# Performance work log

Hardware: AMD Instinct MI355X
Metric: run time of the kernel (lower is better)

Reference implementation:

```python
import math
import jax, jax.numpy as jnp
import numpy as np
from jax import lax

B, L, C_IN = 8, 1024, 64
D_MODEL, N_HEADS, D_FF, E_LAYERS, FACTOR = 512, 8, 2048, 3, 5


def conv1d_circ(x, w):
    # x [B,L,Cin], w [Cout,Cin,K]; torch Conv1d with padding_mode='circular'
    pad = (w.shape[-1] - 1) // 2
    xp = jnp.pad(x, ((0, 0), (pad, pad), (0, 0)), mode='wrap')
    return lax.conv_general_dilated(xp, jnp.transpose(w, (2, 1, 0)), (1,), 'VALID',
                                    dimension_numbers=('NWC', 'WIO', 'NWC'))


def pos_emb(Lq, d):
    pos = jnp.arange(Lq, dtype=jnp.float32)[:, None]
    div = jnp.exp(jnp.arange(0, d, 2, dtype=jnp.float32) * (-math.log(10000.0) / d))
    pe = jnp.zeros((Lq, d), dtype=jnp.float32)
    pe = pe.at[:, 0::2].set(jnp.sin(pos * div)).at[:, 1::2].set(jnp.cos(pos * div))
    return pe


def layer_norm(x, g, b, eps=1e-5):
    m = x.mean(-1, keepdims=True)
    v = ((x - m) ** 2).mean(-1, keepdims=True)
    return (x - m) / jnp.sqrt(v + eps) * g + b


def prob_attention(Q, K, V, rkey):
    # ProbSparse self-attention (mask_flag=False). Q,K,V: [B,H,L,D]
    Bq, H, Lq, D = Q.shape
    U = min(FACTOR * int(math.ceil(math.log(Lq))), Lq)  # sample_k == n_top since L_Q == L_K
    idx = jax.random.randint(rkey, (Lq, U), 0, Lq)       # per-query sampled key indices
    Ks = jnp.take(K, idx, axis=2)                        # [B,H,L,U,D]
    QKs = jnp.einsum('bhld,bhlud->bhlu', Q, Ks)          # sampled scores
    M = QKs.max(-1) - QKs.sum(-1) / Lq                   # sparsity measure (sum / L_K)
    _, top = lax.top_k(M, U)                             # [B,H,U] top-u query indices
    Qr = jnp.take_along_axis(Q, top[..., None], axis=2)  # [B,H,U,D]
    scores = jnp.einsum('bhud,bhld->bhul', Qr, K) * (1.0 / math.sqrt(D))
    attn = jax.nn.softmax(scores, axis=-1)
    upd = jnp.einsum('bhul,bhld->bhud', attn, V)
    # initial context = mean of V broadcast over queries; scatter updates at top-u
    ctx = jnp.broadcast_to(V.mean(axis=2, keepdims=True), (Bq, H, Lq, D))
    bi = jnp.arange(Bq)[:, None, None]
    hi = jnp.arange(H)[None, :, None]
    ctx = ctx.at[bi, hi, top].set(upd)
    return ctx


def attn_block(x, Wq, bq, Wk, bk, Wv, bv, Wo, bo, rkey):
    Bq, Lq, Dm = x.shape
    Dh = Dm // N_HEADS
    q = (x @ Wq.T + bq).reshape(Bq, Lq, N_HEADS, Dh).transpose(0, 2, 1, 3)
    k = (x @ Wk.T + bk).reshape(Bq, Lq, N_HEADS, Dh).transpose(0, 2, 1, 3)
    v = (x @ Wv.T + bv).reshape(Bq, Lq, N_HEADS, Dh).transpose(0, 2, 1, 3)
    ctx = prob_attention(q, k, v, rkey)
    out = ctx.transpose(0, 2, 1, 3).reshape(Bq, Lq, Dm)
    return out @ Wo.T + bo


def distil_conv(x, w, b, g, be):
    # Conv1d(k=3, circular) -> BatchNorm1d (batch stats) -> ELU -> MaxPool1d(3,2,1)
    y = conv1d_circ(x, w) + b
    mu = y.mean((0, 1))
    var = ((y - mu) ** 2).mean((0, 1))
    y = (y - mu) / jnp.sqrt(var + 1e-5) * g + be
    y = jax.nn.elu(y)
    y = lax.reduce_window(y, -jnp.inf, lax.max, (1, 3, 1), (1, 2, 1),
                          ((0, 0), (1, 1), (0, 0)))
    return y


def forward(x_enc, tok_w, Wq, bq, Wk, bk, Wv, bv, Wo, bo, c1w, c1b, c2w, c2b,
            n1g, n1b, n2g, n2b, dcw, dcb, bng, bnb, fng, fnb):
    x = x_enc + 1e-10
    x = conv1d_circ(x, tok_w) + pos_emb(x.shape[1], D_MODEL)  # embedding (dropout=0)
    for l in range(E_LAYERS):
        rkey = jax.random.fold_in(jax.random.key(42), l)
        x = x + attn_block(x, Wq[l], bq[l], Wk[l], bk[l], Wv[l], bv[l], Wo[l], bo[l], rkey)
        y = x = layer_norm(x, n1g[l], n1b[l])
        y = jax.nn.relu(y @ c1w[l].T + c1b[l])   # Conv1d k=1 == linear
        y = y @ c2w[l].T + c2b[l]
        x = layer_norm(x + y, n2g[l], n2b[l])
        if l < E_LAYERS - 1:
            x = distil_conv(x, dcw[l], dcb[l], bng[l], bnb[l])
    x = layer_norm(x, fng, fnb)
    return x.mean(axis=1)  # [B, D_MODEL]


def setup_inputs() -> dict:
    key = jax.random.key(0)
    ks = jax.random.split(key, 12)
    s = 0.02
    E = E_LAYERS
    return {
        'x_enc': jax.random.normal(ks[0], (B, L, C_IN), jnp.float32),
        'tok_w': jax.random.normal(ks[1], (D_MODEL, C_IN, 3), jnp.float32) * s,
        'Wq': jax.random.normal(ks[2], (E, D_MODEL, D_MODEL), jnp.float32) * s,
        'bq': jnp.zeros((E, D_MODEL), jnp.float32),
        'Wk': jax.random.normal(ks[3], (E, D_MODEL, D_MODEL), jnp.float32) * s,
        'bk': jnp.zeros((E, D_MODEL), jnp.float32),
        'Wv': jax.random.normal(ks[4], (E, D_MODEL, D_MODEL), jnp.float32) * s,
        'bv': jnp.zeros((E, D_MODEL), jnp.float32),
        'Wo': jax.random.normal(ks[5], (E, D_MODEL, D_MODEL), jnp.float32) * s,
        'bo': jnp.zeros((E, D_MODEL), jnp.float32),
        'c1w': jax.random.normal(ks[6], (E, D_FF, D_MODEL), jnp.float32) * s,
        'c1b': jnp.zeros((E, D_FF), jnp.float32),
        'c2w': jax.random.normal(ks[7], (E, D_MODEL, D_FF), jnp.float32) * s,
        'c2b': jnp.zeros((E, D_MODEL), jnp.float32),
        'n1g': jnp.ones((E, D_MODEL), jnp.float32),
        'n1b': jnp.zeros((E, D_MODEL), jnp.float32),
        'n2g': jnp.ones((E, D_MODEL), jnp.float32),
        'n2b': jnp.zeros((E, D_MODEL), jnp.float32),
        'dcw': jax.random.normal(ks[8], (E - 1, D_MODEL, D_MODEL, 3), jnp.float32) * s,
        'dcb': jnp.zeros((E - 1, D_MODEL), jnp.float32),
        'bng': jnp.ones((E - 1, D_MODEL), jnp.float32),
        'bnb': jnp.zeros((E - 1, D_MODEL), jnp.float32),
        'fng': jnp.ones((D_MODEL,), jnp.float32),
        'fnb': jnp.zeros((D_MODEL,), jnp.float32),
    }


def reference(x_enc, tok_w, Wq, bq, Wk, bk, Wv, bv, Wo, bo, c1w, c1b, c2w, c2b,
              n1g, n1b, n2g, n2b, dcw, dcb, bng, bnb, fng, fnb):
    return forward(x_enc, tok_w, Wq, bq, Wk, bk, Wv, bv, Wo, bo, c1w, c1b, c2w, c2b,
                   n1g, n1b, n2g, n2b, dcw, dcb, bng, bnb, fng, fnb)
```

## Files before the change

kernel.cpp:

```cpp
#include <hip/hip_runtime.h>
#include <hip/hip_bf16.h>
#include <math.h>

typedef __hip_bfloat16 bf16;
typedef short bf16x8 __attribute__((ext_vector_type(8)));
typedef float f32x4 __attribute__((ext_vector_type(4)));

__device__ inline short f2bs(float x) {
  bf16 h = __float2bfloat16(x);
  return *reinterpret_cast<short*>(&h);
}

__device__ inline void gload16(const bf16* g, bf16* l) {
  __builtin_amdgcn_global_load_lds(
      (const __attribute__((address_space(1))) unsigned int*)g,
      (__attribute__((address_space(3))) unsigned int*)l, 16, 0, 0);
}

__device__ inline void threefry2x32(unsigned k0, unsigned k1,
                                    unsigned x0, unsigned x1,
                                    unsigned& o0, unsigned& o1) {
  unsigned ks[3] = {k0, k1, k0 ^ k1 ^ 0x1BD11BDAu};
  const int rot[2][4] = {{13, 15, 26, 6}, {17, 29, 16, 24}};
  x0 += ks[0];
  x1 += ks[1];
  #pragma unroll
  for (int i = 0; i < 5; i++) {
    const int* r = rot[i & 1];
    #pragma unroll
    for (int j = 0; j < 4; j++) {
      x0 += x1;
      x1 = (x1 << r[j]) | (x1 >> (32 - r[j]));
      x1 ^= x0;
    }
    x0 += ks[(i + 1) % 3];
    x1 += ks[(i + 2) % 3] + (unsigned)(i + 1);
  }
  o0 = x0;
  o1 = x1;
}

__global__ void idx_kernel(int* __restrict__ idx, int L, int U, int layer) {
  int total = L * U, half = total / 2;
  int i = blockIdx.x * blockDim.x + threadIdx.x;
  if (i >= half) return;
  unsigned k0, k1;
  threefry2x32(0u, 42u, 0u, (unsigned)layer, k0, k1);
  unsigned o0, o1;
  threefry2x32(k0, k1, (unsigned)i, (unsigned)(half + i), o0, o1);
  idx[i] = (int)(o0 & (unsigned)(L - 1));
  idx[half + i] = (int)(o1 & (unsigned)(L - 1));
}

__global__ __launch_bounds__(256) void bgemm_g(
    const bf16* __restrict__ A, const bf16* __restrict__ W,
    const float* __restrict__ bias, const float* __restrict__ R, int rmod,
    float* __restrict__ C, bf16* __restrict__ Cb,
    int M, int N, int K, int relu, int outmode) {
  __shared__ bf16 As[2][64 * 64];
  __shared__ bf16 Ws[2][64 * 64];
  int tid = threadIdx.x;
  int lane = tid & 63, w = tid >> 6;
  size_t row0 = (size_t)blockIdx.x * 64, col0 = (size_t)blockIdx.y * 64;
  int srow = w * 16 + (lane >> 3);
  int scol = (((lane & 7) ^ (lane >> 3)) << 4) >> 1;
  const bf16* agA0 = A + (row0 + srow) * K + scol;
  const bf16* agA1 = A + (row0 + srow + 8) * K + scol;
  const bf16* agW0 = W + (col0 + srow) * K + scol;
  const bf16* agW1 = W + (col0 + srow + 8) * K + scol;
  int db0 = (w * 16) * 64;
  int db1 = (w * 16 + 8) * 64;
  int wr = (w >> 1) << 5, wc = (w & 1) << 5;
  int fr = lane & 15;
  int fkb = ((lane >> 4) << 3) << 1;
  f32x4 acc[2][2] = {};
  int nt = K >> 6;
  gload16(agA0, As[0] + db0); gload16(agA1, As[0] + db1);
  gload16(agW0, Ws[0] + db0); gload16(agW1, Ws[0] + db1);
  int cur = 0;
  for (int t = 0; t < nt; t++) {
    __syncthreads();
    if (t + 1 < nt) {
      int ko = (t + 1) << 6;
      gload16(agA0 + ko, As[cur ^ 1] + db0); gload16(agA1 + ko, As[cur ^ 1] + db1);
      gload16(agW0 + ko, Ws[cur ^ 1] + db0); gload16(agW1 + ko, Ws[cur ^ 1] + db1);
    }
    const char* ab = (const char*)As[cur];
    const char* wb = (const char*)Ws[cur];
    bf16x8 af[2][2], bfv[2][2];
    #pragma unroll
    for (int m = 0; m < 2; m++) {
      int row = wr + m * 16 + fr;
      int xr = (row & 7) << 4;
      #pragma unroll
      for (int kk = 0; kk < 2; kk++)
        af[m][kk] = *(const bf16x8*)(ab + row * 128 + ((fkb + kk * 64) ^ xr));
    }
    #pragma unroll
    for (int n = 0; n < 2; n++) {
      int row = wc + n * 16 + fr;
      int xr = (row & 7) << 4;
      #pragma unroll
      for (int kk = 0; kk < 2; kk++)
        bfv[n][kk] = *(const bf16x8*)(wb + row * 128 + ((fkb + kk * 64) ^ xr));
    }
    #pragma unroll
    for (int m = 0; m < 2; m++)
      #pragma unroll
      for (int n = 0; n < 2; n++) {
        acc[m][n] = __builtin_amdgcn_mfma_f32_16x16x32_bf16(af[m][0], bfv[n][0], acc[m][n], 0, 0, 0);
        acc[m][n] = __builtin_amdgcn_mfma_f32_16x16x32_bf16(af[m][1], bfv[n][1], acc[m][n], 0, 0, 0);
      }
    cur ^= 1;
  }
  int cr = (lane >> 4) << 2;
  int cc0 = lane & 15;
  #pragma unroll
  for (int m = 0; m < 2; m++) {
    #pragma unroll
    for (int n = 0; n < 2; n++) {
      #pragma unroll
      for (int r = 0; r < 4; r++) {
        size_t rr = row0 + wr + m * 16 + cr + r;
        size_t cc = col0 + wc + n * 16 + cc0;
        float v = acc[m][n][r];
        if (bias) v += bias[cc];
        if (R) v += rmod ? R[(rr % rmod) * N + cc] : R[rr * N + cc];
        if (relu) v = fmaxf(v, 0.f);
        if (outmode != 2) C[rr * N + cc] = v;
        if (outmode) Cb[rr * N + cc] = __float2bfloat16(v);
      }
    }
  }
}

__global__ void castw_kernel(const float* __restrict__ wq, const float* __restrict__ wk,
                             const float* __restrict__ wv, const float* __restrict__ wo,
                             const float* __restrict__ c1, const float* __restrict__ c2,
                             bf16* __restrict__ wqkv, bf16* __restrict__ wob,
                             bf16* __restrict__ c1b, bf16* __restrict__ c2b) {
  int i = blockIdx.x * 256 + threadIdx.x;
  if (i >= 786432) return;
  const float* s;
  bf16* d;
  int j;
  if (i < 196608) {
    s = (i < 65536) ? wq : (i < 131072) ? wk : wv;
    float4 v = ((const float4*)s)[i & 65535];
    d = wqkv + (size_t)i * 4;
    d[0] = __float2bfloat16(v.x); d[1] = __float2bfloat16(v.y);
    d[2] = __float2bfloat16(v.z); d[3] = __float2bfloat16(v.w);
    return;
  }
  if (i < 262144) { s = wo; j = i - 196608; d = wob + (size_t)j * 4; }
  else if (i < 524288) { s = c1; j = i - 262144; d = c1b + (size_t)j * 4; }
  else { s = c2; j = i - 524288; d = c2b + (size_t)j * 4; }
  float4 v = ((const float4*)s)[j];
  d[0] = __float2bfloat16(v.x); d[1] = __float2bfloat16(v.y);
  d[2] = __float2bfloat16(v.z); d[3] = __float2bfloat16(v.w);
}

__global__ void catb3_kernel(const float* __restrict__ a, const float* __restrict__ b,
                             const float* __restrict__ c, float* __restrict__ d) {
  int i = blockIdx.x * 256 + threadIdx.x;
  if (i >= 1536) return;
  d[i] = (i < 512) ? a[i] : (i < 1024) ? b[i - 512] : c[i - 1024];
}

__global__ void wperm_kernel(const float* __restrict__ w, bf16* __restrict__ wcol) {
  int i = blockIdx.x * 256 + threadIdx.x;
  if (i >= 512 * 1536) return;
  int o = i / 1536, r = i % 1536, k = r / 512, c = r % 512;
  wcol[i] = __float2bfloat16(w[o * 1536 + c * 3 + k]);
}

__global__ void tokperm_kernel(const float* __restrict__ w, bf16* __restrict__ d) {
  int i = blockIdx.x * 256 + threadIdx.x;
  if (i >= 512 * 192) return;
  int o = i / 192, r = i % 192, k = r / 64, c = r % 64;
  d[i] = __float2bfloat16(w[o * 192 + c * 3 + k]);
}

__global__ void pe_kernel(float* __restrict__ PE) {
  int t = blockIdx.x, o = threadIdx.x;
  int i2 = o >> 1;
  float div = expf((float)(2 * i2) * (-9.210340371976184f / 512.f));
  float ang = (float)t * div;
  PE[t * 512 + o] = (o & 1) ? cosf(ang) : sinf(ang);
}

__global__ void im2col_e_kernel(const float* __restrict__ x, bf16* __restrict__ d,
                                int B, int L) {
  size_t i = (size_t)blockIdx.x * 256 + threadIdx.x;
  if (i >= (size_t)B * L * 192) return;
  int j = (int)(i % 192);
  size_t row = i / 192;
  int k = j >> 6, c = j & 63;
  int t = (int)(row % L), b = (int)(row / L);
  int ts = (t - 1 + k) & (L - 1);
  d[i] = __float2bfloat16(x[((size_t)(b * L + ts)) * 64 + c] + 1e-10f);
}

__global__ __launch_bounds__(256) void sparsity_kernel(
    const float* __restrict__ QKV, const int* __restrict__ idx,
    float* __restrict__ M, int B, int H, int L, int U) {
  int tpb = L >> 2;
  int xcd = blockIdx.x & 7, slot = blockIdx.x >> 3;
  int bh = xcd + ((slot / tpb) << 3);
  int tb = slot % tpb;
  int wave = threadIdx.x >> 6;
  int t = tb * 4 + wave;
  int lane = threadIdx.x & 63;
  int h = bh & 7, b = bh >> 3;
  int ul = lane >> 3;
  int j = lane & 7;
  const float* qrow = QKV + ((size_t)(b * L + t)) * 1536 + h * 64 + j * 8;
  float4 qa = *(const float4*)qrow;
  float4 qb = *(const float4*)(qrow + 4);
  const float* kbase = QKV + (size_t)b * L * 1536 + 512 + h * 64 + j * 8;
  const int* irow = idx + t * U;
  float mx = -INFINITY, sm = 0.f;
  int iters = (U + 7) >> 3;
  for (int i = 0; i < iters; i++) {
    int u = i * 8 + ul;
    bool valid = (u < U);
    int kt = valid ? irow[u] : 0;
    const float* kr = kbase + (size_t)kt * 1536;
    float4 ka = *(const float4*)kr;
    float4 kb = *(const float4*)(kr + 4);
    float part = qa.x * ka.x + qa.y * ka.y + qa.z * ka.z + qa.w * ka.w +
                 qb.x * kb.x + qb.y * kb.y + qb.z * kb.z + qb.w * kb.w;
    #pragma unroll
    for (int off = 1; off < 8; off <<= 1) part += __shfl_xor(part, off);
    if (valid) { mx = fmaxf(mx, part); sm += part; }
  }
  #pragma unroll
  for (int off = 8; off < 64; off <<= 1) {
    mx = fmaxf(mx, __shfl_xor(mx, off));
    sm += __shfl_xor(sm, off);
  }
  if (lane == 0) M[(size_t)bh * L + t] = mx - sm / (float)L;
}

__global__ __launch_bounds__(1024) void topk_kernel(
    const float* __restrict__ M, int* __restrict__ top, int L, int U) {
  __shared__ float wv[16];
  __shared__ int wi[16];
  __shared__ int best_s;
  int bh = blockIdx.x, tid = threadIdx.x;
  int lane = tid & 63, w = tid >> 6;
  float v = (tid < L) ? M[(size_t)bh * L + tid] : -INFINITY;
  int myt = tid;
  for (int it = 0; it < U; it++) {
    float bv = v;
    int bi = myt;
    #pragma unroll
    for (int off = 32; off; off >>= 1) {
      float ov = __shfl_xor(bv, off);
      int oi = __shfl_xor(bi, off);
      if (ov > bv || (ov == bv && oi < bi)) { bv = ov; bi = oi; }
    }
    if (lane == 0) { wv[w] = bv; wi[w] = bi; }
    __syncthreads();
    if (w == 0) {
      float v2 = (lane < 16) ? wv[lane] : -INFINITY;
      int i2 = (lane < 16) ? wi[lane] : 0x7fffffff;
      #pragma unroll
      for (int off = 8; off; off >>= 1) {
        float ov = __shfl_xor(v2, off);
        int oi = __shfl_xor(i2, off);
        if (ov > v2 || (ov == v2 && oi < i2)) { v2 = ov; i2 = oi; }
      }
      if (lane == 0) { best_s = i2; top[bh * U + it] = i2; }
    }
    __syncthreads();
    if (myt == best_s) v = -INFINITY;
  }
}

__global__ __launch_bounds__(512) void vmean_part_kernel(
    const float* __restrict__ QKV, float* __restrict__ VP, int L, int segs) {
  int b = blockIdx.x, s = blockIdx.y, c = threadIdx.x;
  int per = L / segs;
  const float* vb = QKV + ((size_t)(b * L + s * per)) * 1536 + 1024 + c;
  float acc = 0.f;
  for (int t = 0; t < per; t++) acc += vb[(size_t)t * 1536];
  VP[((size_t)(b * segs + s)) * 512 + c] = acc;
}

__global__ void vmean_reduce_kernel(const float* __restrict__ VP, float* __restrict__ Vmean,
                                    int segs, int L) {
  int i = blockIdx.x * 256 + threadIdx.x;
  if (i >= 8 * 512) return;
  int b = i >> 9, c = i & 511;
  float acc = 0.f;
  for (int s = 0; s < segs; s++) acc += VP[((size_t)(b * segs + s)) * 512 + c];
  Vmean[i] = acc / (float)L;
}

__global__ void bcast_ctx_kernel(const float* __restrict__ Vmean, bf16* __restrict__ ATTb,
                                 int B, int L) {
  size_t i = (size_t)blockIdx.x * 256 + threadIdx.x;
  if (i >= (size_t)B * L * 512) return;
  int c = (int)(i % 512);
  int b = (int)(i / ((size_t)512 * L));
  ATTb[i] = __float2bfloat16(Vmean[b * 512 + c]);
}

__global__ __launch_bounds__(256) void attn_mfma_kernel(
    const float* __restrict__ QKV, const int* __restrict__ top,
    bf16* __restrict__ ATTb, int B, int H, int L, int U) {
  __shared__ short q_lds[64 * 72];
  __shared__ short k_lds[64 * 72];
  __shared__ short vt_lds[64 * 72];
  __shared__ short p_lds[4][16 * 72];
  int bh = blockIdx.x;
  int h = bh & 7, b = bh >> 3;
  int tid = threadIdx.x;
  int lane = tid & 63, w = tid >> 6;
  int r = tid >> 2, q4 = tid & 3, c0 = q4 << 4;
  int fr = lane & 15, fk = (lane >> 4) << 3, g = lane >> 4;

  {
    short tmp[16];
    if (r < U) {
      int tq = top[bh * U + r];
      const float* src = QKV + ((size_t)(b * L + tq)) * 1536 + h * 64 + c0;
      #pragma unroll
      for (int i = 0; i < 4; i++) {
        float4 v = ((const float4*)src)[i];
        tmp[i * 4 + 0] = f2bs(v.x); tmp[i * 4 + 1] = f2bs(v.y);
        tmp[i * 4 + 2] = f2bs(v.z); tmp[i * 4 + 3] = f2bs(v.w);
      }
    } else {
      #pragma unroll
      for (int i = 0; i < 16; i++) tmp[i] = 0;
    }
    *(bf16x8*)&q_lds[r * 72 + c0] = *(bf16x8*)&tmp[0];
    *(bf16x8*)&q_lds[r * 72 + c0 + 8] = *(bf16x8*)&tmp[8];
  }
  __syncthreads();
  bf16x8 aq0 = *(const bf16x8*)&q_lds[(w * 16 + fr) * 72 + fk];
  bf16x8 aq1 = *(const bf16x8*)&q_lds[(w * 16 + fr) * 72 + 32 + fk];

  f32x4 ctx[4] = {};
  float m_run[4], l_run[4];
  #pragma unroll
  for (int i = 0; i < 4; i++) { m_run[i] = -INFINITY; l_run[i] = 0.f; }

  for (int t0 = 0; t0 < L; t0 += 64) {
    __syncthreads();
    {
      const float* ks = QKV + ((size_t)(b * L + t0 + r)) * 1536 + 512 + h * 64 + c0;
      const float* vs = ks + 512;
      short kt[16];
      #pragma unroll
      for (int i = 0; i < 4; i++) {
        float4 v = ((const float4*)ks)[i];
        kt[i * 4 + 0] = f2bs(v.x); kt[i * 4 + 1] = f2bs(v.y);
        kt[i * 4 + 2] = f2bs(v.z); kt[i * 4 + 3] = f2bs(v.w);
      }
      *(bf16x8*)&k_lds[r * 72 + c0] = *(bf16x8*)&kt[0];
      *(bf16x8*)&k_lds[r * 72 + c0 + 8] = *(bf16x8*)&kt[8];
      #pragma unroll
      for (int i = 0; i < 4; i++) {
        float4 v = ((const float4*)vs)[i];
        vt_lds[(c0 + i * 4 + 0) * 72 + r] = f2bs(v.x);
        vt_lds[(c0 + i * 4 + 1) * 72 + r] = f2bs(v.y);
        vt_lds[(c0 + i * 4 + 2) * 72 + r] = f2bs(v.z);
        vt_lds[(c0 + i * 4 + 3) * 72 + r] = f2bs(v.w);
      }
    }
    __syncthreads();
    f32x4 s[4];
    #pragma unroll
    for (int n = 0; n < 4; n++) {
      bf16x8 b0 = *(const bf16x8*)&k_lds[(n * 16 + fr) * 72 + fk];
      bf16x8 b1 = *(const bf16x8*)&k_lds[(n * 16 + fr) * 72 + 32 + fk];
      f32x4 z = {};
      z = __builtin_amdgcn_mfma_f32_16x16x32_bf16(aq0, b0, z, 0, 0, 0);
      s[n] = __builtin_amdgcn_mfma_f32_16x16x32_bf16(aq1, b1, z, 0, 0, 0);
    }
    #pragma unroll
    for (int n = 0; n < 4; n++)
      #pragma unroll
      for (int rg = 0; rg < 4; rg++) s[n][rg] *= 0.125f;
    #pragma unroll
    for (int rg = 0; rg < 4; rg++) {
      float tm = fmaxf(fmaxf(s[0][rg], s[1][rg]), fmaxf(s[2][rg], s[3][rg]));
      #pragma unroll
      for (int off = 1; off < 16; off <<= 1) tm = fmaxf(tm, __shfl_xor(tm, off));
      float mnew = fmaxf(m_run[rg], tm);
      float sc_old = expf(m_run[rg] - mnew);
      float rowsum = 0.f;
      #pragma unroll
      for (int n = 0; n < 4; n++) {
        float p = expf(s[n][rg] - mnew);
        s[n][rg] = p;
        rowsum += p;
      }
      #pragma unroll
      for (int off = 1; off < 16; off <<= 1) rowsum += __shfl_xor(rowsum, off);
      l_run[rg] = l_run[rg] * sc_old + rowsum;
      m_run[rg] = mnew;
      #pragma unroll
      for (int nd = 0; nd < 4; nd++) ctx[nd][rg] *= sc_old;
    }
    short* pw = p_lds[w];
    #pragma unroll
    for (int n = 0; n < 4; n++)
      #pragma unroll
      for (int rg = 0; rg < 4; rg++)
        pw[(g * 4 + rg) * 72 + n * 16 + fr] = f2bs(s[n][rg]);
    bf16x8 pa0 = *(const bf16x8*)&pw[fr * 72 + fk];
    bf16x8 pa1 = *(const bf16x8*)&pw[fr * 72 + 32 + fk];
    #pragma unroll
    for (int nd = 0; nd < 4; nd++) {
      bf16x8 v0 = *(const bf16x8*)&vt_lds[(nd * 16 + fr) * 72 + fk];
      bf16x8 v1 = *(const bf16x8*)&vt_lds[(nd * 16 + fr) * 72 + 32 + fk];
      ctx[nd] = __builtin_amdgcn_mfma_f32_16x16x32_bf16(pa0, v0, ctx[nd], 0, 0, 0);
      ctx[nd] = __builtin_amdgcn_mfma_f32_16x16x32_bf16(pa1, v1, ctx[nd], 0, 0, 0);
    }
  }
  #pragma unroll
  for (int rg = 0; rg < 4; rg++) {
    int qq = w * 16 + g * 4 + rg;
    if (qq < U) {
      int tq = top[bh * U + qq];
      float inv = 1.f / l_run[rg];
      #pragma unroll
      for (int nd = 0; nd < 4; nd++) {
        int d = nd * 16 + fr;
        ATTb[((size_t)(b * L + tq)) * 512 + h * 64 + d] =
            __float2bfloat16(ctx[nd][rg] * inv);
      }
    }
  }
}

__global__ __launch_bounds__(256) void ln_kernel(
    const float* __restrict__ Xin, const float* __restrict__ g,
    const float* __restrict__ bta, float* __restrict__ Xout,
    bf16* __restrict__ Xoutb, int rows) {
  __shared__ float part[8];
  int r = blockIdx.x, tid = threadIdx.x;
  int lane = tid & 63, w = tid >> 6;
  const float* xr = Xin + (size_t)r * 512;
  float v0 = xr[tid], v1 = xr[tid + 256];
  float s = v0 + v1;
  #pragma unroll
  for (int off = 1; off < 64; off <<= 1) s += __shfl_xor(s, off);
  if (lane == 0) part[w] = s;
  __syncthreads();
  float mean = (part[0] + part[1] + part[2] + part[3]) * (1.f / 512.f);
  float d0 = v0 - mean, d1 = v1 - mean;
  float q = d0 * d0 + d1 * d1;
  #pragma unroll
  for (int off = 1; off < 64; off <<= 1) q += __shfl_xor(q, off);
  if (lane == 0) part[4 + w] = q;
  __syncthreads();
  float var = (part[4] + part[5] + part[6] + part[7]) * (1.f / 512.f);
  float rs = rsqrtf(var + 1e-5f);
  float o0 = d0 * rs * g[tid] + bta[tid];
  float o1 = d1 * rs * g[tid + 256] + bta[tid + 256];
  float* out = Xout + (size_t)r * 512;
  out[tid] = o0;
  out[tid + 256] = o1;
  if (Xoutb) {
    Xoutb[(size_t)r * 512 + tid] = __float2bfloat16(o0);
    Xoutb[(size_t)r * 512 + tid + 256] = __float2bfloat16(o1);
  }
}

__global__ void im2col_kernel(const float* __restrict__ X, bf16* __restrict__ XCOL,
                              int B, int L) {
  size_t i = (size_t)blockIdx.x * 256 + threadIdx.x;
  size_t total = (size_t)B * L * 1536;
  if (i >= total) return;
  int c = (int)(i % 512);
  int k = (int)((i / 512) % 3);
  size_t row = i / 1536;
  int t = (int)(row % L), b = (int)(row / L);
  int ts = (t - 1 + k + L) % L;
  XCOL[i] = __float2bfloat16(X[((size_t)(b * L + ts)) * 512 + c]);
}

__global__ void zero_kernel(float* p, int n) {
  int i = blockIdx.x * 256 + threadIdx.x;
  if (i < n) p[i] = 0.f;
}

__global__ __launch_bounds__(256) void bnstat_kernel(
    const float* __restrict__ Y, float* __restrict__ acc, int rows) {
  int tid = threadIdx.x;
  int c0 = tid, c1 = tid + 256;
  float s0 = 0, s1 = 0, q0 = 0, q1 = 0;
  for (int r = blockIdx.x; r < rows; r += gridDim.x) {
    float v0 = Y[(size_t)r * 512 + c0];
    float v1 = Y[(size_t)r * 512 + c1];
    s0 += v0; q0 += v0 * v0;
    s1 += v1; q1 += v1 * v1;
  }
  atomicAdd(&acc[c0], s0);
  atomicAdd(&acc[c1], s1);
  atomicAdd(&acc[512 + c0], q0);
  atomicAdd(&acc[512 + c1], q1);
}

__global__ void bnpool_kernel(const float* __restrict__ Y, const float* __restrict__ acc,
                              const float* __restrict__ g, const float* __restrict__ be,
                              float* __restrict__ Xout, bf16* __restrict__ Xoutb,
                              int B, int L, int rows) {
  int Lout = L / 2;
  size_t i = (size_t)blockIdx.x * 256 + threadIdx.x;
  if (i >= (size_t)B * Lout * 512) return;
  int c = (int)(i % 512);
  size_t orow = i / 512;
  int to = (int)(orow % Lout), b = (int)(orow / Lout);
  float mu = acc[c] / (float)rows;
  float var = acc[512 + c] / (float)rows - mu * mu;
  float rs = rsqrtf(var + 1e-5f) * g[c];
  float mx = -INFINITY;
  #pragma unroll
  for (int dj = -1; dj <= 1; dj++) {
    int j = 2 * to + dj;
    if (j < 0 || j >= L) continue;
    float v = (Y[((size_t)(b * L + j)) * 512 + c] - mu) * rs + be[c];
    v = v > 0.f ? v : expm1f(v);
    mx = fmaxf(mx, v);
  }
  Xout[i] = mx;
  Xoutb[i] = __float2bfloat16(mx);
}

__global__ void meanrows_part_kernel(const float* __restrict__ Xin, float* __restrict__ MP,
                                     int L, int segs) {
  int b = blockIdx.x, s = blockIdx.y, d = threadIdx.x;
  int per = L / segs;
  const float* base = Xin + ((size_t)(b * L + s * per)) * 512 + d;
  float acc = 0.f;
  for (int t = 0; t < per; t++) acc += base[(size_t)t * 512];
  MP[((size_t)(b * segs + s)) * 512 + d] = acc;
}

__global__ void meanrows_red_kernel(const float* __restrict__ MP, float* __restrict__ out,
                                    int segs, int L) {
  int i = blockIdx.x * 256 + threadIdx.x;
  if (i >= 8 * 512) return;
  int b = i >> 9, c = i & 511;
  float acc = 0.f;
  for (int s = 0; s < segs; s++) acc += MP[((size_t)(b * segs + s)) * 512 + c];
  out[i] = acc / (float)L;
}

extern "C" void kernel_launch(void* const* d_in, const int* in_sizes, int n_in,
                              void* d_out, int out_size, void* d_ws, size_t ws_size,
                              hipStream_t stream) {
  const float* x_enc = (const float*)d_in[0];
  const float* tok_w = (const float*)d_in[1];
  const float* Wq = (const float*)d_in[2];
  const float* bq = (const float*)d_in[3];
  const float* Wk = (const float*)d_in[4];
  const float* bk = (const float*)d_in[5];
  const float* Wv = (const float*)d_in[6];
  const float* bv = (const float*)d_in[7];
  const float* Wo = (const float*)d_in[8];
  const float* bo = (const float*)d_in[9];
  const float* c1w = (const float*)d_in[10];
  const float* c1b = (const float*)d_in[11];
  const float* c2w = (const float*)d_in[12];
  const float* c2b = (const float*)d_in[13];
  const float* n1g = (const float*)d_in[14];
  const float* n1b = (const float*)d_in[15];
  const float* n2g = (const float*)d_in[16];
  const float* n2b = (const float*)d_in[17];
  const float* dcw = (const float*)d_in[18];
  const float* dcb = (const float*)d_in[19];
  const float* bng = (const float*)d_in[20];
  const float* bnb = (const float*)d_in[21];
  const float* fng = (const float*)d_in[22];
  const float* fnb = (const float*)d_in[23];

  const int B = 8, H = 8;
  const size_t NX = 4194304;

  float* ws = (float*)d_ws;
  float* X    = ws;
  float* XLN  = ws + NX;
  float* QKVf = ws + 2 * NX;
  bf16* H2b   = (bf16*)(ws + 2 * NX);
  float* Yc   = ws + 2 * NX;
  bf16* XCOLb = (bf16*)(ws + 4 * NX);
  bf16* INb   = (bf16*)(ws + 5 * NX);
  bf16* ATTb  = (bf16*)(ws + 5 * NX + NX / 2);
  float* WB   = ws + 6 * NX;
  bf16* WQKVb = (bf16*)(WB);
  bf16* Wob  = (bf16*)(WB + 393216);
  bf16* c1wb = (bf16*)(WB + 524288);
  bf16* c2wb = (bf16*)(WB + 1048576);
  bf16* wcvb = (bf16*)(WB + 1572864);
  bf16* tokwb = (bf16*)(WB + 1966080);
  float* PE   = WB + 2015232;
  float* MBUF = PE + 524288;
  float* VMEAN = MBUF + 65536;
  float* BNACC = VMEAN + 4096;
  int* IDX = (int*)(BNACC + 1024);
  int* TOP = IDX + 35840;
  float* VPART = (float*)(TOP + 2240);
  float* BQKV = VPART + 131072;

  pe_kernel<<<1024, 512, 0, stream>>>(PE);
  tokperm_kernel<<<(512 * 192 + 255) / 256, 256, 0, stream>>>(tok_w, tokwb);
  im2col_e_kernel<<<(int)(((size_t)B * 1024 * 192 + 255) / 256), 256, 0, stream>>>(
      x_enc, INb, B, 1024);
  bgemm_g<<<dim3(128, 8), 256, 0, stream>>>(INb, tokwb, nullptr, PE, 1024,
                                            X, INb, 8192, 512, 192, 0, 1);

  int L = 1024;
  for (int l = 0; l < 3; l++) {
    int U = (L == 256) ? 30 : 35;
    int rows = B * L;
    dim3 g64(rows / 64, 8);

    castw_kernel<<<3072, 256, 0, stream>>>(
        Wq + (size_t)l * 262144, Wk + (size_t)l * 262144, Wv + (size_t)l * 262144,
        Wo + (size_t)l * 262144, c1w + (size_t)l * 1048576, c2w + (size_t)l * 1048576,
        WQKVb, Wob, c1wb, c2wb);
    catb3_kernel<<<6, 256, 0, stream>>>(bq + l * 512, bk + l * 512, bv + l * 512, BQKV);
    if (l < 2)
      wperm_kernel<<<3072, 256, 0, stream>>>(dcw + (size_t)l * 786432, wcvb);

    bgemm_g<<<dim3(rows / 64, 24), 256, 0, stream>>>(
        INb, WQKVb, BQKV, nullptr, 0, QKVf, nullptr, rows, 1536, 512, 0, 0);

    int half = L * U / 2;
    idx_kernel<<<(half + 255) / 256, 256, 0, stream>>>(IDX, L, U, l);
    sparsity_kernel<<<(B * H * L) / 4, 256, 0, stream>>>(QKVf, IDX, MBUF, B, H, L, U);
    topk_kernel<<<B * H, 1024, 0, stream>>>(MBUF, TOP, L, U);
    vmean_part_kernel<<<dim3(B, 32), 512, 0, stream>>>(QKVf, VPART, L, 32);
    vmean_reduce_kernel<<<16, 256, 0, stream>>>(VPART, VMEAN, 32, L);
    bcast_ctx_kernel<<<(rows * 512) / 256, 256, 0, stream>>>(VMEAN, ATTb, B, L);
    attn_mfma_kernel<<<B * H, 256, 0, stream>>>(QKVf, TOP, ATTb, B, H, L, U);

    bgemm_g<<<g64, 256, 0, stream>>>(ATTb, Wob, bo + l * 512, X, 0,
                                     X, nullptr, rows, 512, 512, 0, 0);
    ln_kernel<<<rows, 256, 0, stream>>>(X, n1g + l * 512, n1b + l * 512, XLN, INb, rows);
    bgemm_g<<<dim3(rows / 64, 32), 256, 0, stream>>>(
        INb, c1wb, c1b + l * 2048, nullptr, 0, nullptr, H2b, rows, 2048, 512, 1, 2);
    bgemm_g<<<g64, 256, 0, stream>>>(H2b, c2wb, c2b + l * 512, XLN, 0,
                                     X, nullptr, rows, 512, 2048, 0, 0);
    ln_kernel<<<rows, 256, 0, stream>>>(X, n2g + l * 512, n2b + l * 512, X, nullptr, rows);

    if (l < 2) {
      im2col_kernel<<<(int)(((size_t)rows * 1536) / 256), 256, 0, stream>>>(X, XCOLb, B, L);
      bgemm_g<<<g64, 256, 0, stream>>>(XCOLb, wcvb, dcb + l * 512, nullptr, 0,
                                       Yc, nullptr, rows, 512, 1536, 0, 0);
      zero_kernel<<<4, 256, 0, stream>>>(BNACC, 1024);
      bnstat_kernel<<<128, 256, 0, stream>>>(Yc, BNACC, rows);
      bnpool_kernel<<<(rows / 2 * 512) / 256, 256, 0, stream>>>(
          Yc, BNACC, bng + l * 512, bnb + l * 512, X, INb, B, L, rows);
      L >>= 1;
    }
  }

  int rowsF = B * L;
  ln_kernel<<<rowsF, 256, 0, stream>>>(X, fng, fnb, XLN, nullptr, rowsF);
  meanrows_part_kernel<<<dim3(8, 8), 512, 0, stream>>>(XLN, VPART, L, 8);
  meanrows_red_kernel<<<16, 256, 0, stream>>>(VPART, (float*)d_out, 8, L);
}
```

Baseline: 877.2 us.

## Split ProbSparse attention over key chunks with a separate combine kernel

The attention kernel used to launch only B*H=64 blocks, each sweeping every key, which leaves most CUs idle. It now splits the key range into SPLIT chunks (8 for L>=512, 4 otherwise). Each chunk writes an unnormalized context plus its running max and sum to scratch space reused from the XLN buffer. A new combine kernel merges the chunks flash-decoding style and scatters the result into ATTb, at the cost of an extra launch and some scratch traffic.

```diff
diff --git a/kernel.cpp b/kernel.cpp
--- a/kernel.cpp
+++ b/kernel.cpp
@@ -307,14 +307,17 @@
   ATTb[i] = __float2bfloat16(Vmean[b * 512 + c]);
 }
 
-__global__ __launch_bounds__(256) void attn_mfma_kernel(
+__global__ __launch_bounds__(256) void attn_partial_kernel(
     const float* __restrict__ QKV, const int* __restrict__ top,
-    bf16* __restrict__ ATTb, int B, int H, int L, int U) {
+    float* __restrict__ PCTX, float* __restrict__ PML,
+    int B, int H, int L, int U, int SPLIT) {
   __shared__ short q_lds[64 * 72];
   __shared__ short k_lds[64 * 72];
   __shared__ short vt_lds[64 * 72];
   __shared__ short p_lds[4][16 * 72];
-  int bh = blockIdx.x;
+  int bh = blockIdx.x / SPLIT;
+  int sp = blockIdx.x % SPLIT;
+  int KS = L / SPLIT;
   int h = bh & 7, b = bh >> 3;
   int tid = threadIdx.x;
   int lane = tid & 63, w = tid >> 6;
@@ -348,7 +351,7 @@
   #pragma unroll
   for (int i = 0; i < 4; i++) { m_run[i] = -INFINITY; l_run[i] = 0.f; }
 
-  for (int t0 = 0; t0 < L; t0 += 64) {
+  for (int t0 = sp * KS; t0 < sp * KS + KS; t0 += 64) {
     __syncthreads();
     {
       const float* ks = QKV + ((size_t)(b * L + t0 + r)) * 1536 + 512 + h * 64 + c0;
@@ -426,16 +429,40 @@
   for (int rg = 0; rg < 4; rg++) {
     int qq = w * 16 + g * 4 + rg;
     if (qq < U) {
-      int tq = top[bh * U + qq];
-      float inv = 1.f / l_run[rg];
-      #pragma unroll
-      for (int nd = 0; nd < 4; nd++) {
-        int d = nd * 16 + fr;
-        ATTb[((size_t)(b * L + tq)) * 512 + h * 64 + d] =
-            __float2bfloat16(ctx[nd][rg] * inv);
+      size_t base = ((size_t)bh * SPLIT + sp) * 64 + qq;
+      #pragma unroll
+      for (int nd = 0; nd < 4; nd++)
+        PCTX[base * 64 + nd * 16 + fr] = ctx[nd][rg];
+      if (fr == 0) {
+        PML[base * 2] = m_run[rg];
+        PML[base * 2 + 1] = l_run[rg];
       }
     }
   }
+}
+
+__global__ __launch_bounds__(256) void attn_combine_kernel(
+    const float* __restrict__ PCTX, const float* __restrict__ PML,
+    const int* __restrict__ top, bf16* __restrict__ ATTb,
+    int B, int H, int L, int U, int SPLIT) {
+  int bh = blockIdx.x;
+  int row = blockIdx.y * 4 + (threadIdx.x >> 6);
+  int d = threadIdx.x & 63;
+  if (row >= U) return;
+  int h = bh & 7, b = bh >> 3;
+  float mstar = -INFINITY;
+  for (int sp = 0; sp < SPLIT; sp++)
+    mstar = fmaxf(mstar, PML[(((size_t)bh * SPLIT + sp) * 64 + row) * 2]);
+  float lstar = 0.f, cacc = 0.f;
+  for (int sp = 0; sp < SPLIT; sp++) {
+    size_t base = ((size_t)bh * SPLIT + sp) * 64 + row;
+    float m = PML[base * 2], lv = PML[base * 2 + 1];
+    float wgt = expf(m - mstar);
+    lstar += lv * wgt;
+    cacc += PCTX[base * 64 + d] * wgt;
+  }
+  int tq = top[bh * U + row];
+  ATTb[((size_t)(b * L + tq)) * 512 + h * 64 + d] = __float2bfloat16(cacc / lstar);
 }
 
 __global__ __launch_bounds__(256) void ln_kernel(
@@ -587,6 +614,8 @@
   float* ws = (float*)d_ws;
   float* X    = ws;
   float* XLN  = ws + NX;
+  float* PCTX = XLN;
+  float* PML  = XLN + 2097152;
   float* QKVf = ws + 2 * NX;
   bf16* H2b   = (bf16*)(ws + 2 * NX);
   float* Yc   = ws + 2 * NX;
@@ -619,6 +648,7 @@
   int L = 1024;
   for (int l = 0; l < 3; l++) {
     int U = (L == 256) ? 30 : 35;
+    int SPLIT = (L >= 512) ? 8 : 4;
     int rows = B * L;
     dim3 g64(rows / 64, 8);
 
@@ -640,7 +670,10 @@
     vmean_part_kernel<<<dim3(B, 32), 512, 0, stream>>>(QKVf, VPART, L, 32);
     vmean_reduce_kernel<<<16, 256, 0, stream>>>(VPART, VMEAN, 32, L);
     bcast_ctx_kernel<<<(rows * 512) / 256, 256, 0, stream>>>(VMEAN, ATTb, B, L);
-    attn_mfma_kernel<<<B * H, 256, 0, stream>>>(QKVf, TOP, ATTb, B, H, L, U);
+    attn_partial_kernel<<<B * H * SPLIT, 256, 0, stream>>>(
+        QKVf, TOP, PCTX, PML, B, H, L, U, SPLIT);
+    attn_combine_kernel<<<dim3(B * H, (U + 3) / 4), 256, 0, stream>>>(
+        PCTX, PML, TOP, ATTb, B, H, L, U, SPLIT);
 
     bgemm_g<<<g64, 256, 0, stream>>>(ATTb, Wob, bo + l * 512, X, 0,
                                      X, nullptr, rows, 512, 512, 0, 0);
```

After: 830.1 us. 1.06x faster.
